# Performance work log

Measured on AMD Instinct MI355X. Metric: run time of the kernel, lower is better.

## Reference

```python
import jax, jax.numpy as jnp
import numpy as np

B, N, C, H = 2, 2048, 768, 12
D = C // H            # head_dim = 64
SCALE = D ** -0.5
QMAX_8 = 127.0        # int8 symmetric weights/activations (BIT_TYPE_W / BIT_TYPE_A)
LOG_QMAX = 15.0       # uint4 log-domain softmax (BIT_TYPE_S)


def setup_inputs() -> dict:
    key = jax.random.key(0)
    k0, k1, k2 = jax.random.split(key, 3)
    x = jax.random.normal(k0, (B, N, C), jnp.float32)
    w_qkv = jax.random.normal(k1, (3 * C, C), jnp.float32) * 0.02
    b_qkv = jnp.zeros((3 * C,), jnp.float32)
    w_out = jax.random.normal(k2, (C, C), jnp.float32) * 0.02
    b_out = jnp.zeros((C,), jnp.float32)
    return {"x": x, "w_qkv": w_qkv, "b_qkv": b_qkv, "w_out": w_out, "b_out": b_out}


def fake_quant_sym(t):
    """Symmetric per-tensor int8 fake-quantize (quantize->dequantize), STE for grads."""
    s = jnp.max(jnp.abs(t)) / QMAX_8 + 1e-8
    deq = jnp.clip(jnp.round(t / s), -QMAX_8, QMAX_8) * s
    return t + jax.lax.stop_gradient(deq - t)


def log_int_softmax(attn):
    """Log-int-softmax: softmax then 4-bit log2 quantization, attn_q = 2^{-round(-log2 p)}."""
    p = jax.nn.softmax(attn, axis=-1)
    lg = jnp.clip(jnp.round(-jnp.log2(jnp.maximum(p, 2.0 ** -24))), 0.0, LOG_QMAX)
    q = jnp.exp2(-lg)
    return p + jax.lax.stop_gradient(q - p)


def reference(x, w_qkv, b_qkv, w_out, b_out):
    # QLinear: fake-quantized weight GEMM
    qkv = x @ fake_quant_sym(w_qkv).T + b_qkv            # [B,N,3C]
    qkv = fake_quant_sym(qkv)                            # qact_qkv
    qkv = qkv.reshape(B, N, 3, H, D).transpose(2, 0, 3, 1, 4)  # [3,B,H,N,D]
    q, k, v = qkv[0], qkv[1], qkv[2]
    attn = jnp.einsum("bhnd,bhmd->bhnm", q, k) * SCALE   # [B,H,N,N]
    attn = fake_quant_sym(attn)                          # qact_attn
    p = log_int_softmax(attn)
    o = jnp.einsum("bhnm,bhmd->bhnd", p, v)              # [B,H,N,D]
    o = o.transpose(0, 2, 1, 3).reshape(B, N, C)
    out = o @ fake_quant_sym(w_out).T + b_out            # out_proj (QLinear)
    out = fake_quant_sym(out)                            # qact_out
    return out
```

## Files before the change

### kernel.cpp

```cpp
#include <hip/hip_runtime.h>

#define NB 2
#define NN 2048
#define NC 768
#define NH 12
#define ND 64
#define ROWS (NB * NN)
#define K3C (3 * NC)
#define NHEADS (NB * NH)
#define ATTN_SCALE 0.125f

typedef __attribute__((ext_vector_type(8))) short s16x8;
typedef __attribute__((ext_vector_type(4))) float f32x4;
typedef __attribute__((ext_vector_type(2))) unsigned int u32x2;

__device__ __forceinline__ float qsc(const unsigned* u) {
    return __uint_as_float(*u) / 127.0f + 1e-8f;
}
__device__ __forceinline__ float fq(float t, float s) {
    return fminf(fmaxf(rintf(t / s), -127.0f), 127.0f) * s;
}
__device__ __forceinline__ float qcode(float t, float s) {
    return fminf(fmaxf(rintf(t / s), -127.0f), 127.0f);
}
__device__ __forceinline__ short bfbits(float f) {
    return (short)(__float_as_uint(f) >> 16);
}
__device__ __forceinline__ ushort bf_rne(float x) {
    unsigned u = __float_as_uint(x);
    return (ushort)((u + 0x7fffu + ((u >> 16) & 1u)) >> 16);
}

__global__ __launch_bounds__(256) void maxabs_kernel(const float* __restrict__ x,
                                                     long long n, unsigned* out) {
    float m = 0.0f;
    long long stride4 = (long long)gridDim.x * blockDim.x * 4;
    for (long long j = ((long long)blockIdx.x * blockDim.x + threadIdx.x) * 4; j < n; j += stride4) {
        float4 v = *(const float4*)(x + j);
        m = fmaxf(m, fmaxf(fmaxf(fabsf(v.x), fabsf(v.y)), fmaxf(fabsf(v.z), fabsf(v.w))));
    }
    for (int off = 32; off > 0; off >>= 1) m = fmaxf(m, __shfl_down(m, off, 64));
    __shared__ float sm[4];
    int lane = threadIdx.x & 63, w = threadIdx.x >> 6;
    if (lane == 0) sm[w] = m;
    __syncthreads();
    if (threadIdx.x == 0) {
        float mm = fmaxf(fmaxf(sm[0], sm[1]), fmaxf(sm[2], sm[3]));
        atomicMax(out, __float_as_uint(mm));
    }
}

__global__ __launch_bounds__(256) void quant_kernel(const float* in, float* out,
                                                    long long n, const unsigned* umax) {
    float s = qsc(umax);
    long long stride4 = (long long)gridDim.x * blockDim.x * 4;
    for (long long j = ((long long)blockIdx.x * blockDim.x + threadIdx.x) * 4; j < n; j += stride4) {
        float4 v = *(const float4*)(in + j);
        v.x = fq(v.x, s); v.y = fq(v.y, s); v.z = fq(v.z, s); v.w = fq(v.w, s);
        *(float4*)(out + j) = v;
    }
}

__global__ __launch_bounds__(256) void quantcodes_kernel(const float* __restrict__ in,
                                                         ushort* __restrict__ codes,
                                                         long long n,
                                                         const unsigned* __restrict__ umax) {
    float s = qsc(umax);
    long long stride8 = (long long)gridDim.x * blockDim.x * 8;
    for (long long j = ((long long)blockIdx.x * blockDim.x + threadIdx.x) * 8; j < n; j += stride8) {
        float4 a = *(const float4*)(in + j);
        float4 b = *(const float4*)(in + j + 4);
        s16x8 o;
        o[0] = bfbits(qcode(a.x, s)); o[1] = bfbits(qcode(a.y, s));
        o[2] = bfbits(qcode(a.z, s)); o[3] = bfbits(qcode(a.w, s));
        o[4] = bfbits(qcode(b.x, s)); o[5] = bfbits(qcode(b.y, s));
        o[6] = bfbits(qcode(b.z, s)); o[7] = bfbits(qcode(b.w, s));
        *(s16x8*)(codes + j) = o;
    }
}

__global__ __launch_bounds__(256) void split3_kernel(const float* __restrict__ in,
                                                     ushort* __restrict__ xs,
                                                     long long n) {
    long long stride8 = (long long)gridDim.x * blockDim.x * 8;
    for (long long j = ((long long)blockIdx.x * blockDim.x + threadIdx.x) * 8; j < n; j += stride8) {
        long long row = j / NC, col = j % NC;
        s16x8 h, m, l;
#pragma unroll
        for (int i = 0; i < 8; i += 4) {
            float4 v = *(const float4*)(in + j + i);
            float vv[4] = {v.x, v.y, v.z, v.w};
#pragma unroll
            for (int t = 0; t < 4; ++t) {
                ushort hb = bf_rne(vv[t]);
                float hf = __uint_as_float(((unsigned)hb) << 16);
                float r1 = vv[t] - hf;
                ushort mb = bf_rne(r1);
                float mf = __uint_as_float(((unsigned)mb) << 16);
                h[i + t] = (short)hb;
                m[i + t] = (short)mb;
                l[i + t] = (short)bf_rne(r1 - mf);
            }
        }
        ushort* dst = xs + row * (3 * NC) + col;
        *(s16x8*)(dst) = h;
        *(s16x8*)(dst + NC) = m;
        *(s16x8*)(dst + 2 * NC) = l;
    }
}

__global__ __launch_bounds__(256) void gemm3_mfma_kernel(const ushort* __restrict__ As,
                                                         const ushort* __restrict__ Bc,
                                                         const float* __restrict__ bias,
                                                         float* __restrict__ Cm, int Nn,
                                                         const unsigned* __restrict__ uB,
                                                         unsigned* __restrict__ uC) {
    __shared__ ushort ah[128 * 64], am[128 * 64], al[128 * 64], bs[128 * 64];
    __shared__ float redmx[4];
    const float sB = qsc(uB);
    const int tid = threadIdx.x, l = tid & 63, w = tid >> 6;
    const int row0 = blockIdx.y * 128, col0 = blockIdx.x * 128;
    const int wr = w >> 1, wc = w & 1;
    f32x4 acc[4][4];
#pragma unroll
    for (int m = 0; m < 4; ++m)
#pragma unroll
        for (int n = 0; n < 4; ++n) acc[m][n] = (f32x4){0.f, 0.f, 0.f, 0.f};

    const int sr = tid >> 1, sh = (tid & 1) << 5;
    const int su = sh >> 3, s7 = sr & 7;

    for (int k0 = 0; k0 < NC; k0 += 64) {
        __syncthreads();
        {
            const ushort* ph = As + (size_t)(row0 + sr) * (3 * NC) + k0 + sh;
            ushort* dsts[3] = {ah + sr * 64, am + sr * 64, al + sr * 64};
#pragma unroll
            for (int pl = 0; pl < 3; ++pl) {
                const ushort* p = ph + pl * NC;
                s16x8 t0 = *(const s16x8*)(p),      t1 = *(const s16x8*)(p + 8);
                s16x8 t2 = *(const s16x8*)(p + 16), t3 = *(const s16x8*)(p + 24);
                ushort* d = dsts[pl];
                *(s16x8*)(d + (((su | 0) ^ s7) << 3)) = t0;
                *(s16x8*)(d + (((su | 1) ^ s7) << 3)) = t1;
                *(s16x8*)(d + (((su | 2) ^ s7) << 3)) = t2;
                *(s16x8*)(d + (((su | 3) ^ s7) << 3)) = t3;
            }
            const ushort* pb = Bc + (size_t)(col0 + sr) * NC + k0 + sh;
            s16x8 b0 = *(const s16x8*)(pb),      b1 = *(const s16x8*)(pb + 8);
            s16x8 b2 = *(const s16x8*)(pb + 16), b3 = *(const s16x8*)(pb + 24);
            ushort* brow = bs + sr * 64;
            *(s16x8*)(brow + (((su | 0) ^ s7) << 3)) = b0;
            *(s16x8*)(brow + (((su | 1) ^ s7) << 3)) = b1;
            *(s16x8*)(brow + (((su | 2) ^ s7) << 3)) = b2;
            *(s16x8*)(brow + (((su | 3) ^ s7) << 3)) = b3;
        }
        __syncthreads();
#pragma unroll
        for (int ks = 0; ks < 2; ++ks) {
            s16x8 bf[4];
#pragma unroll
            for (int n = 0; n < 4; ++n) {
                int br = wc * 64 + n * 16 + (l & 15);
                bf[n] = *(s16x8*)(bs + br * 64 + ((((ks << 2) + (l >> 4)) ^ (br & 7)) << 3));
            }
#pragma unroll
            for (int m = 0; m < 4; ++m) {
                int ar = wr * 64 + m * 16 + (l & 15);
                int ao = ar * 64 + ((((ks << 2) + (l >> 4)) ^ (ar & 7)) << 3);
                s16x8 af = *(s16x8*)(ah + ao);
                s16x8 mf_ = *(s16x8*)(am + ao);
                s16x8 ef = *(s16x8*)(al + ao);
#pragma unroll
                for (int n = 0; n < 4; ++n) {
                    acc[m][n] = __builtin_amdgcn_mfma_f32_16x16x32_bf16(af, bf[n], acc[m][n], 0, 0, 0);
                    acc[m][n] = __builtin_amdgcn_mfma_f32_16x16x32_bf16(mf_, bf[n], acc[m][n], 0, 0, 0);
                    acc[m][n] = __builtin_amdgcn_mfma_f32_16x16x32_bf16(ef, bf[n], acc[m][n], 0, 0, 0);
                }
            }
        }
    }
    float mx = 0.0f;
#pragma unroll
    for (int n = 0; n < 4; ++n) {
        int col = col0 + wc * 64 + n * 16 + (l & 15);
        float bv = bias[col];
#pragma unroll
        for (int m = 0; m < 4; ++m) {
            int grow = row0 + wr * 64 + m * 16 + ((l >> 4) << 2);
#pragma unroll
            for (int r = 0; r < 4; ++r) {
                float v = fmaf(sB, acc[m][n][r], bv);
                Cm[(size_t)(grow + r) * Nn + col] = v;
                mx = fmaxf(mx, fabsf(v));
            }
        }
    }
    for (int msk = 1; msk < 64; msk <<= 1) mx = fmaxf(mx, __shfl_xor(mx, msk, 64));
    if (l == 0) redmx[w] = mx;
    __syncthreads();
    if (tid == 0)
        atomicMax(uC, __float_as_uint(fmaxf(fmaxf(redmx[0], redmx[1]), fmaxf(redmx[2], redmx[3]))));
}

__device__ __forceinline__ void stage_k_tile(const ushort* __restrict__ src,
                                             ushort* lds, int tid) {
    int row = tid >> 2, u0 = (tid & 3) << 1, r7 = row & 7;
    const ushort* p = src + (size_t)row * K3C + (u0 << 3);
    s16x8 t0 = *(const s16x8*)(p);
    s16x8 t1 = *(const s16x8*)(p + 8);
    *(s16x8*)(lds + row * 64 + ((u0 ^ r7) << 3)) = t0;
    *(s16x8*)(lds + row * 64 + (((u0 | 1) ^ r7) << 3)) = t1;
}

__device__ __forceinline__ void stage_vT_tile(const ushort* __restrict__ src,
                                              ushort* lds, int tid) {
    int j = tid >> 2, d0 = (tid & 3) << 4;
    const ushort* p = src + (size_t)j * K3C + d0;
    s16x8 a = *(const s16x8*)(p);
    s16x8 b = *(const s16x8*)(p + 8);
    int jo = j >> 3, jl = j & 7;
#pragma unroll
    for (int t = 0; t < 8; ++t) {
        int d = d0 + t;
        lds[d * 64 + ((jo ^ (d & 7)) << 3) + jl] = (ushort)a[t];
    }
#pragma unroll
    for (int t = 0; t < 8; ++t) {
        int d = d0 + 8 + t;
        lds[d * 64 + ((jo ^ (d & 7)) << 3) + jl] = (ushort)b[t];
    }
}

__global__ __launch_bounds__(256) void attn_maxdot_kernel(const ushort* __restrict__ codes,
                                                          unsigned* __restrict__ umaxdot) {
    __shared__ ushort kt[64 * 64];
    __shared__ float red[4];
    int bh = blockIdx.y, b = bh / NH, h = bh % NH;
    int i0 = blockIdx.x * 64;
    int tid = threadIdx.x, l = tid & 63, w = tid >> 6;
    int qr = l & 15, g = l >> 4;

    const ushort* qp = codes + (size_t)(b * NN + i0 + w * 16 + qr) * K3C + h * ND + (g << 3);
    s16x8 qf0 = *(const s16x8*)(qp);
    s16x8 qf1 = *(const s16x8*)(qp + 32);

    const ushort* kbase = codes + (size_t)(b * NN) * K3C + NC + h * ND;
    float md = 0.0f;
    for (int st = 0; st < NN / 64; ++st) {
        __syncthreads();
        stage_k_tile(kbase + (size_t)st * 64 * K3C, kt, tid);
        __syncthreads();
#pragma unroll
        for (int jt = 0; jt < 4; ++jt) {
            int row = (jt << 4) + qr;
            f32x4 acc = {0.f, 0.f, 0.f, 0.f};
            s16x8 kf0 = *(s16x8*)(kt + row * 64 + (((g    ) ^ (row & 7)) << 3));
            s16x8 kf1 = *(s16x8*)(kt + row * 64 + (((g + 4) ^ (row & 7)) << 3));
            acc = __builtin_amdgcn_mfma_f32_16x16x32_bf16(kf0, qf0, acc, 0, 0, 0);
            acc = __builtin_amdgcn_mfma_f32_16x16x32_bf16(kf1, qf1, acc, 0, 0, 0);
#pragma unroll
            for (int r = 0; r < 4; ++r) md = fmaxf(md, fabsf(acc[r]));
        }
    }
    for (int m = 1; m < 64; m <<= 1) md = fmaxf(md, __shfl_xor(md, m, 64));
    if (l == 0) red[w] = md;
    __syncthreads();
    if (tid == 0)
        atomicMax(umaxdot, __float_as_uint(fmaxf(fmaxf(red[0], red[1]), fmaxf(red[2], red[3]))));
}

__global__ __launch_bounds__(256) void attn_fused_kernel(const ushort* __restrict__ codes,
                                                         const unsigned* __restrict__ uq,
                                                         const unsigned* __restrict__ umaxdot,
                                                         float* __restrict__ O) {
    __shared__ ushort kt[64 * 64];
    __shared__ ushort vt[64 * 64];
    __shared__ ushort ps[4][16 * 64];
    int bh = blockIdx.y, b = bh / NH, h = bh % NH;
    int i0 = blockIdx.x * 64;
    int tid = threadIdx.x, l = tid & 63, w = tid >> 6;
    int qr = l & 15, g = l >> 4;
    float s = qsc(uq);
    float cf = s * s * ATTN_SCALE;
    float sa = __uint_as_float(*umaxdot) * cf / 127.0f + 1e-8f;
    float rr = cf / sa;
    float kk = sa * 1.44269504088896340736f;

    const ushort* qp = codes + (size_t)(b * NN + i0 + w * 16 + qr) * K3C + h * ND + (g << 3);
    s16x8 qf0 = *(const s16x8*)(qp);
    s16x8 qf1 = *(const s16x8*)(qp + 32);

    const ushort* kbase = codes + (size_t)(b * NN) * K3C + NC + h * ND;
    const ushort* vbase = codes + (size_t)(b * NN) * K3C + 2 * NC + h * ND;

    float U = 0.0f;
    for (int st = 0; st < NN / 64; ++st) {
        __syncthreads();
        stage_k_tile(kbase + (size_t)st * 64 * K3C, kt, tid);
        __syncthreads();
#pragma unroll
        for (int jt = 0; jt < 4; ++jt) {
            int row = (jt << 4) + qr;
            f32x4 acc = {0.f, 0.f, 0.f, 0.f};
            s16x8 kf0 = *(s16x8*)(kt + row * 64 + (((g    ) ^ (row & 7)) << 3));
            s16x8 kf1 = *(s16x8*)(kt + row * 64 + (((g + 4) ^ (row & 7)) << 3));
            acc = __builtin_amdgcn_mfma_f32_16x16x32_bf16(kf0, qf0, acc, 0, 0, 0);
            acc = __builtin_amdgcn_mfma_f32_16x16x32_bf16(kf1, qf1, acc, 0, 0, 0);
#pragma unroll
            for (int r = 0; r < 4; ++r) {
                float m = rintf(acc[r] * rr);
                U += exp2f(kk * m);
            }
        }
    }
    U += __shfl_xor(U, 16, 64);
    U += __shfl_xor(U, 32, 64);
    float lu = log2f(U);

    f32x4 oacc[4];
#pragma unroll
    for (int dt = 0; dt < 4; ++dt) oacc[dt] = (f32x4){0.f, 0.f, 0.f, 0.f};
    ushort* myps = (ushort*)ps[w];
    for (int st = 0; st < NN / 64; ++st) {
        __syncthreads();
        stage_k_tile(kbase + (size_t)st * 64 * K3C, kt, tid);
        stage_vT_tile(vbase + (size_t)st * 64 * K3C, vt, tid);
        __syncthreads();
#pragma unroll
        for (int jt = 0; jt < 4; ++jt) {
            int row = (jt << 4) + qr;
            f32x4 acc = {0.f, 0.f, 0.f, 0.f};
            s16x8 kf0 = *(s16x8*)(kt + row * 64 + (((g    ) ^ (row & 7)) << 3));
            s16x8 kf1 = *(s16x8*)(kt + row * 64 + (((g + 4) ^ (row & 7)) << 3));
            acc = __builtin_amdgcn_mfma_f32_16x16x32_bf16(kf0, qf0, acc, 0, 0, 0);
            acc = __builtin_amdgcn_mfma_f32_16x16x32_bf16(kf1, qf1, acc, 0, 0, 0);
            int lg[4];
#pragma unroll
            for (int r = 0; r < 4; ++r) {
                float m = rintf(acc[r] * rr);
                float tt = lu - kk * m;
                lg[r] = (int)fminf(fmaxf(rintf(tt), 0.0f), 15.0f);
            }
            unsigned w0 = (unsigned)(((127 - lg[0]) << 7) | ((127 - lg[1]) << 23));
            unsigned w1 = (unsigned)(((127 - lg[2]) << 7) | ((127 - lg[3]) << 23));
            int off = qr * 64 + (((jt << 4) + ((g >> 1) << 3)) ^ ((qr & 7) << 3)) + ((g & 1) << 2);
            *(u32x2*)(myps + off) = (u32x2){w0, w1};
        }
#pragma unroll
        for (int kc = 0; kc < 2; ++kc) {
            int poff = qr * 64 + (((kc << 5) + (g << 3)) ^ ((qr & 7) << 3));
            s16x8 pf = *(s16x8*)(myps + poff);
#pragma unroll
            for (int dt = 0; dt < 4; ++dt) {
                int drow = (dt << 4) + qr;
                s16x8 vf = *(s16x8*)(vt + drow * 64 + ((((kc << 2) + g) ^ (drow & 7)) << 3));
                oacc[dt] = __builtin_amdgcn_mfma_f32_16x16x32_bf16(pf, vf, oacc[dt], 0, 0, 0);
            }
        }
    }
#pragma unroll
    for (int dt = 0; dt < 4; ++dt)
#pragma unroll
        for (int r = 0; r < 4; ++r) {
            int orow = i0 + w * 16 + (g << 2) + r;
            O[(size_t)(b * NN + orow) * NC + h * ND + (dt << 4) + qr] = s * oacc[dt][r];
        }
}

extern "C" void kernel_launch(void* const* d_in, const int* in_sizes, int n_in,
                              void* d_out, int out_size, void* d_ws, size_t ws_size,
                              hipStream_t stream) {
    const float* x      = (const float*)d_in[0];
    const float* w_qkv  = (const float*)d_in[1];
    const float* b_qkv  = (const float*)d_in[2];
    const float* w_out  = (const float*)d_in[3];
    const float* b_out  = (const float*)d_in[4];
    float* out = (float*)d_out;

    char* ws = (char*)d_ws;
    unsigned* u = (unsigned*)ws;
    const size_t qkvB = (size_t)ROWS * K3C * 4;
    float*  qkv     = (float*)(ws + 256);
    float*  out_tmp = (float*)(ws + 256);
    ushort* woc     = (ushort*)(ws + 256 + 16 * 1024 * 1024);
    char*   codesRg = ws + 256 + qkvB;
    ushort* codes   = (ushort*)codesRg;
    ushort* xsplit  = (ushort*)codesRg;
    ushort* wqc     = (ushort*)d_out;

    hipMemsetAsync(u, 0, 64, stream);

    maxabs_kernel<<<512, 256, 0, stream>>>(w_qkv, (long long)K3C * NC, u + 0);
    maxabs_kernel<<<512, 256, 0, stream>>>(w_out, (long long)NC * NC, u + 1);
    quantcodes_kernel<<<512, 256, 0, stream>>>(w_qkv, wqc, (long long)K3C * NC, u + 0);

    split3_kernel<<<1024, 256, 0, stream>>>(x, xsplit, (long long)ROWS * NC);
    gemm3_mfma_kernel<<<dim3(K3C / 128, ROWS / 128), 256, 0, stream>>>(xsplit, wqc, b_qkv,
                                                                       qkv, K3C, u + 0, u + 2);
    quantcodes_kernel<<<2048, 256, 0, stream>>>(qkv, codes, (long long)ROWS * K3C, u + 2);
    quantcodes_kernel<<<256, 256, 0, stream>>>(w_out, woc, (long long)NC * NC, u + 1);

    attn_maxdot_kernel<<<dim3(NN / 64, NHEADS), 256, 0, stream>>>(codes, u + 3);
    attn_fused_kernel<<<dim3(NN / 64, NHEADS), 256, 0, stream>>>(codes, u + 2, u + 3, out);

    split3_kernel<<<1024, 256, 0, stream>>>(out, xsplit, (long long)ROWS * NC);
    gemm3_mfma_kernel<<<dim3(NC / 128, ROWS / 128), 256, 0, stream>>>(xsplit, woc, b_out,
                                                                      out_tmp, NC, u + 1, u + 4);
    quant_kernel<<<1024, 256, 0, stream>>>(out_tmp, out, (long long)ROWS * NC, u + 4);
}
```

Before: 363.1 us.

## Double-buffer K/V LDS tiles in attention, swizzle GEMM blocks and vT layout

```diff
diff --git a/kernel.cpp b/kernel.cpp
--- a/kernel.cpp
+++ b/kernel.cpp
@@ -8,6 +8,7 @@
 #define ROWS (NB * NN)
 #define K3C (3 * NC)
 #define NHEADS (NB * NH)
+#define NT 32
 #define ATTN_SCALE 0.125f
 
 typedef __attribute__((ext_vector_type(8))) short s16x8;
@@ -119,7 +120,11 @@
     __shared__ float redmx[4];
     const float sB = qsc(uB);
     const int tid = threadIdx.x, l = tid & 63, w = tid >> 6;
-    const int row0 = blockIdx.y * 128, col0 = blockIdx.x * 128;
+    const int nbx = Nn >> 7;
+    const int nwg = nbx * (ROWS >> 7);
+    int bid = blockIdx.y * nbx + blockIdx.x;
+    int swz = (bid & 7) * (nwg >> 3) + (bid >> 3);
+    const int row0 = (swz / nbx) * 128, col0 = (swz % nbx) * 128;
     const int wr = w >> 1, wc = w & 1;
     f32x4 acc[4][4];
 #pragma unroll
@@ -223,18 +228,18 @@
 #pragma unroll
     for (int t = 0; t < 8; ++t) {
         int d = d0 + t;
-        lds[d * 64 + ((jo ^ (d & 7)) << 3) + jl] = (ushort)a[t];
+        lds[d * 64 + (((jo ^ (d & 7)) ^ ((d >> 3) & 7)) << 3) + jl] = (ushort)a[t];
     }
 #pragma unroll
     for (int t = 0; t < 8; ++t) {
         int d = d0 + 8 + t;
-        lds[d * 64 + ((jo ^ (d & 7)) << 3) + jl] = (ushort)b[t];
+        lds[d * 64 + (((jo ^ (d & 7)) ^ ((d >> 3) & 7)) << 3) + jl] = (ushort)b[t];
     }
 }
 
 __global__ __launch_bounds__(256) void attn_maxdot_kernel(const ushort* __restrict__ codes,
                                                           unsigned* __restrict__ umaxdot) {
-    __shared__ ushort kt[64 * 64];
+    __shared__ ushort kt[2][64 * 64];
     __shared__ float red[4];
     int bh = blockIdx.y, b = bh / NH, h = bh % NH;
     int i0 = blockIdx.x * 64;
@@ -246,17 +251,18 @@
     s16x8 qf1 = *(const s16x8*)(qp + 32);
 
     const ushort* kbase = codes + (size_t)(b * NN) * K3C + NC + h * ND;
+    stage_k_tile(kbase, kt[0], tid);
     float md = 0.0f;
-    for (int st = 0; st < NN / 64; ++st) {
+    for (int st = 0; st < NT; ++st) {
         __syncthreads();
-        stage_k_tile(kbase + (size_t)st * 64 * K3C, kt, tid);
-        __syncthreads();
+        if (st + 1 < NT) stage_k_tile(kbase + (size_t)(st + 1) * 64 * K3C, kt[(st + 1) & 1], tid);
+        const ushort* ktc = kt[st & 1];
 #pragma unroll
         for (int jt = 0; jt < 4; ++jt) {
             int row = (jt << 4) + qr;
             f32x4 acc = {0.f, 0.f, 0.f, 0.f};
-            s16x8 kf0 = *(s16x8*)(kt + row * 64 + (((g    ) ^ (row & 7)) << 3));
-            s16x8 kf1 = *(s16x8*)(kt + row * 64 + (((g + 4) ^ (row & 7)) << 3));
+            s16x8 kf0 = *(s16x8*)(ktc + row * 64 + (((g    ) ^ (row & 7)) << 3));
+            s16x8 kf1 = *(s16x8*)(ktc + row * 64 + (((g + 4) ^ (row & 7)) << 3));
             acc = __builtin_amdgcn_mfma_f32_16x16x32_bf16(kf0, qf0, acc, 0, 0, 0);
             acc = __builtin_amdgcn_mfma_f32_16x16x32_bf16(kf1, qf1, acc, 0, 0, 0);
 #pragma unroll
@@ -274,8 +280,8 @@
                                                          const unsigned* __restrict__ uq,
                                                          const unsigned* __restrict__ umaxdot,
                                                          float* __restrict__ O) {
-    __shared__ ushort kt[64 * 64];
-    __shared__ ushort vt[64 * 64];
+    __shared__ ushort kt[2][64 * 64];
+    __shared__ ushort vt[2][64 * 64];
     __shared__ ushort ps[4][16 * 64];
     int bh = blockIdx.y, b = bh / NH, h = bh % NH;
     int i0 = blockIdx.x * 64;
@@ -294,17 +300,18 @@
     const ushort* kbase = codes + (size_t)(b * NN) * K3C + NC + h * ND;
     const ushort* vbase = codes + (size_t)(b * NN) * K3C + 2 * NC + h * ND;
 
+    stage_k_tile(kbase, kt[0], tid);
     float U = 0.0f;
-    for (int st = 0; st < NN / 64; ++st) {
+    for (int st = 0; st < NT; ++st) {
         __syncthreads();
-        stage_k_tile(kbase + (size_t)st * 64 * K3C, kt, tid);
-        __syncthreads();
+        if (st + 1 < NT) stage_k_tile(kbase + (size_t)(st + 1) * 64 * K3C, kt[(st + 1) & 1], tid);
+        const ushort* ktc = kt[st & 1];
 #pragma unroll
         for (int jt = 0; jt < 4; ++jt) {
             int row = (jt << 4) + qr;
             f32x4 acc = {0.f, 0.f, 0.f, 0.f};
-            s16x8 kf0 = *(s16x8*)(kt + row * 64 + (((g    ) ^ (row & 7)) << 3));
-            s16x8 kf1 = *(s16x8*)(kt + row * 64 + (((g + 4) ^ (row & 7)) << 3));
+            s16x8 kf0 = *(s16x8*)(ktc + row * 64 + (((g    ) ^ (row & 7)) << 3));
+            s16x8 kf1 = *(s16x8*)(ktc + row * 64 + (((g + 4) ^ (row & 7)) << 3));
             acc = __builtin_amdgcn_mfma_f32_16x16x32_bf16(kf0, qf0, acc, 0, 0, 0);
             acc = __builtin_amdgcn_mfma_f32_16x16x32_bf16(kf1, qf1, acc, 0, 0, 0);
 #pragma unroll
@@ -322,17 +329,23 @@
 #pragma unroll
     for (int dt = 0; dt < 4; ++dt) oacc[dt] = (f32x4){0.f, 0.f, 0.f, 0.f};
     ushort* myps = (ushort*)ps[w];
-    for (int st = 0; st < NN / 64; ++st) {
+    __syncthreads();
+    stage_k_tile(kbase, kt[0], tid);
+    stage_vT_tile(vbase, vt[0], tid);
+    for (int st = 0; st < NT; ++st) {
         __syncthreads();
-        stage_k_tile(kbase + (size_t)st * 64 * K3C, kt, tid);
-        stage_vT_tile(vbase + (size_t)st * 64 * K3C, vt, tid);
-        __syncthreads();
+        if (st + 1 < NT) {
+            stage_k_tile(kbase + (size_t)(st + 1) * 64 * K3C, kt[(st + 1) & 1], tid);
+            stage_vT_tile(vbase + (size_t)(st + 1) * 64 * K3C, vt[(st + 1) & 1], tid);
+        }
+        const ushort* ktc = kt[st & 1];
+        const ushort* vtc = vt[st & 1];
 #pragma unroll
         for (int jt = 0; jt < 4; ++jt) {
             int row = (jt << 4) + qr;
             f32x4 acc = {0.f, 0.f, 0.f, 0.f};
-            s16x8 kf0 = *(s16x8*)(kt + row * 64 + (((g    ) ^ (row & 7)) << 3));
-            s16x8 kf1 = *(s16x8*)(kt + row * 64 + (((g + 4) ^ (row & 7)) << 3));
+            s16x8 kf0 = *(s16x8*)(ktc + row * 64 + (((g    ) ^ (row & 7)) << 3));
+            s16x8 kf1 = *(s16x8*)(ktc + row * 64 + (((g + 4) ^ (row & 7)) << 3));
             acc = __builtin_amdgcn_mfma_f32_16x16x32_bf16(kf0, qf0, acc, 0, 0, 0);
             acc = __builtin_amdgcn_mfma_f32_16x16x32_bf16(kf1, qf1, acc, 0, 0, 0);
             int lg[4];
@@ -354,7 +367,8 @@
 #pragma unroll
             for (int dt = 0; dt < 4; ++dt) {
                 int drow = (dt << 4) + qr;
-                s16x8 vf = *(s16x8*)(vt + drow * 64 + ((((kc << 2) + g) ^ (drow & 7)) << 3));
+                s16x8 vf = *(s16x8*)(vtc + drow * 64 +
+                                     (((((kc << 2) + g) ^ (drow & 7)) ^ ((drow >> 3) & 7)) << 3));
                 oacc[dt] = __builtin_amdgcn_mfma_f32_16x16x32_bf16(pf, vf, oacc[dt], 0, 0, 0);
             }
         }
```

Measured after the change: 362.0 us. No clear change (-0.3%).
